# Kernel tuning notes

Measured on AMD Instinct MI355X. Metric: run time of the kernel, lower is better.

## Reference

```python
import jax, jax.numpy as jnp
import numpy as np

B_, S_, DM, DI, N_, R_, K_ = 2, 2048, 256, 512, 16, 32, 4
NB = 4  # 2 forward + 2 backward MambaBlocks


def setup_inputs() -> dict:
    key = jax.random.key(0)
    ks = jax.random.split(key, 16)
    def rn(k, shape, s=0.02):
        return jax.random.normal(k, shape, jnp.float32) * s
    A = jnp.log(jnp.arange(1, N_ + 1, dtype=jnp.float32))  # [N]
    return {
        'x': jax.random.normal(ks[0], (B_, S_, DM), jnp.float32),
        'in_w': rn(ks[1], (NB, DM, 2 * DI)),
        'conv_w': rn(ks[2], (NB, DI, K_), 0.3),
        'conv_b': jnp.zeros((NB, DI), jnp.float32),
        'A_log': jnp.broadcast_to(A, (NB, DI, N_)) + 0.0,
        'xd_w': rn(ks[3], (NB, DI, R_)),
        'xB_w': rn(ks[4], (NB, DI, N_)),
        'xC_w': rn(ks[5], (NB, DI, N_)),
        'dtp_w': rn(ks[6], (NB, R_, DI), R_ ** -0.5),
        'dtp_b': jax.random.uniform(ks[7], (NB, DI), jnp.float32,
                                    minval=jnp.log(0.001), maxval=jnp.log(0.1)),
        'D': jnp.ones((NB, DI), jnp.float32),
        'out_w': rn(ks[8], (NB, DI, DM)),
        'ln_g': jnp.ones((NB, DM), jnp.float32),
        'ln_b': jnp.zeros((NB, DM), jnp.float32),
        'merge_w': rn(ks[9], (2 * DM, DM)),
    }


def _layer_norm(x, g, b, eps=1e-5):
    m = jnp.mean(x, axis=-1, keepdims=True)
    v = jnp.mean(jnp.square(x - m), axis=-1, keepdims=True)
    return (x - m) * jax.lax.rsqrt(v + eps) * g + b


def _ssm_scan(dA, dBx, C):
    # dA, dBx: [B,S,DI,N]; C: [B,S,N] -> y: [B,S,DI]
    def step(h, inp):
        dA_t, dBx_t, C_t = inp
        h = dA_t * h + dBx_t                      # [B,DI,N]
        y = jnp.einsum('bdn,bn->bd', h, C_t)      # [B,DI]
        return h, y
    h0 = jnp.zeros(dA.shape[:1] + dA.shape[2:], dA.dtype)
    _, ys = jax.lax.scan(step, h0, (dA.transpose(1, 0, 2, 3),
                                    dBx.transpose(1, 0, 2, 3),
                                    C.transpose(1, 0, 2)))
    return ys.transpose(1, 0, 2)


def _mamba_block(x, in_w, conv_w, conv_b, A_log, xd_w, xB_w, xC_w,
                 dtp_w, dtp_b, D, out_w, g, b):
    res = x
    xn = _layer_norm(x, g, b)
    xz = xn @ in_w                                # [B,S,2*DI]
    xs, z = jnp.split(xz, 2, axis=-1)
    # causal depthwise conv: left pad K-1 (equals torch pad=K-1 then slice [:S])
    xc = jax.lax.conv_general_dilated(
        xs.transpose(0, 2, 1), conv_w[:, None, :], (1,), [(K_ - 1, 0)],
        dimension_numbers=('NCH', 'OIH', 'NCH'), feature_group_count=DI)
    xc = jax.nn.silu((xc + conv_b[None, :, None]).transpose(0, 2, 1))  # [B,S,DI]
    delta = jax.nn.softplus((xc @ xd_w) @ dtp_w + dtp_b)               # [B,S,DI]
    Bm = xc @ xB_w                                # [B,S,N]
    Cm = xc @ xC_w                                # [B,S,N]
    A = -jnp.exp(A_log)                           # [DI,N]
    dA = jnp.exp(delta[..., None] * A)            # [B,S,DI,N]
    dBx = (delta * xc)[..., None] * Bm[:, :, None, :]
    y = _ssm_scan(dA, dBx, Cm) + D * xc
    return (y * jax.nn.silu(z)) @ out_w + res


def reference(x, in_w, conv_w, conv_b, A_log, xd_w, xB_w, xC_w,
              dtp_w, dtp_b, D, out_w, ln_g, ln_b, merge_w):
    def blk(h, i):
        return _mamba_block(h, in_w[i], conv_w[i], conv_b[i], A_log[i],
                            xd_w[i], xB_w[i], xC_w[i], dtp_w[i], dtp_b[i],
                            D[i], out_w[i], ln_g[i], ln_b[i])
    fwd = blk(blk(x, 0), 1)
    bwd = blk(blk(x[:, ::-1], 2), 3)[:, ::-1]
    return jnp.concatenate([fwd, bwd], axis=-1) @ merge_w
```

## Files before the change

### kernel.cpp

```cpp
#include <hip/hip_runtime.h>

#define S_LEN 2048
#define DINNER 512
#define NCHUNK 64
#define CLEN 32

typedef unsigned short u16;
typedef short bf16x8 __attribute__((ext_vector_type(8)));
typedef unsigned short u16x8 __attribute__((ext_vector_type(8)));
typedef float f32x4 __attribute__((ext_vector_type(4)));

__device__ __forceinline__ float bf2f(u16 u) {
  unsigned int x = ((unsigned int)u) << 16;
  float f; __builtin_memcpy(&f, &x, 4); return f;
}
__device__ __forceinline__ u16 f2bf(float f) {
  unsigned int x; __builtin_memcpy(&x, &f, 4);
  return (u16)((x + 0x7FFFu + ((x >> 16) & 1u)) >> 16);
}
__device__ __forceinline__ float ldw(const void* p, size_t i, int isbf) {
  return isbf ? bf2f(((const u16*)p)[i]) : ((const float*)p)[i];
}
__device__ __forceinline__ float siluf(float x) { return x / (1.f + __expf(-x)); }
__device__ __forceinline__ float softplusf(float x) {
  if (x > 20.f) return x;
  return log1pf(__expf(x));
}

__global__ __launch_bounds__(256) void detect_kernel(const void* __restrict__ x,
                                                     int* __restrict__ flag) {
  __shared__ int cnt;
  if (threadIdx.x == 0) cnt = 0;
  __syncthreads();
  u16 u = ((const u16*)x)[2 * threadIdx.x];
  int e = (u >> 7) & 0xFF;
  if (e >= 0x60 && e <= 0x8F) atomicAdd(&cnt, 1);
  __syncthreads();
  if (threadIdx.x == 0) *flag = (cnt > 128) ? 1 : 0;
}

__global__ __launch_bounds__(256) void apack_kernel(
    const void* __restrict__ A_log, const int* __restrict__ pf, float* __restrict__ Acp)
{
  const int isbf = *pf;
  int idx = blockIdx.x * 256 + threadIdx.x;
  Acp[idx] = -__expf(ldw(A_log, (size_t)idx, isbf));
}

__global__ __launch_bounds__(256) void wpack_kernel(
    const void* __restrict__ src, const int* __restrict__ pf,
    u16* __restrict__ dst, int K, int N)
{
  const int isbf = *pf;
  __shared__ float tile[32][65];
  int nb64 = blockIdx.x, kb = blockIdx.y, mat = blockIdx.z;
  size_t so = (size_t)mat * K * N;
  int tid = threadIdx.x;
  int kk = tid >> 3, nseg = (tid & 7) * 8;
#pragma unroll
  for (int j = 0; j < 8; ++j)
    tile[kk][nseg + j] = ldw(src, so + (size_t)(kb * 32 + kk) * N + nb64 * 64 + nseg + j, isbf);
  __syncthreads();
  int cc = tid >> 6, i0 = (tid & 63) * 8;
  int q = i0 >> 7, nn = (i0 >> 3) & 15;
  u16 outv[8];
#pragma unroll
  for (int j = 0; j < 8; ++j) outv[j] = f2bf(tile[q * 8 + j][cc * 16 + nn]);
  size_t doff = (size_t)mat * K * N + ((size_t)(nb64 * 4 + cc) * (K >> 5) + kb) * 512 + i0;
  *(u16x8*)(dst + doff) = *(const u16x8*)outv;
}

__global__ __launch_bounds__(256) void wpack_cmb_kernel(
    const void* __restrict__ xdw, const void* __restrict__ dtpw,
    const void* __restrict__ xBw, const void* __restrict__ xCw,
    const int* __restrict__ pf, u16* __restrict__ dst)
{
  const int isbf = *pf;
  __shared__ float tile[32][65];
  int nb64 = blockIdx.x, kb = blockIdx.y, mat = blockIdx.z;
  int tid = threadIdx.x;
  if (nb64 < 8) {
    __shared__ float xd[32][33];
    __shared__ float wt[32][65];
    {
      int k = tid >> 3, j0 = (tid & 7) * 4;
#pragma unroll
      for (int j = 0; j < 4; ++j)
        xd[k][j0 + j] = ldw(xdw, (size_t)mat * 16384 + (size_t)(kb * 32 + k) * 32 + j0 + j, isbf);
      int jj = tid >> 3, n0l = (tid & 7) * 8;
#pragma unroll
      for (int n = 0; n < 8; ++n)
        wt[jj][n0l + n] = ldw(dtpw, (size_t)mat * 16384 + (size_t)jj * 512 + nb64 * 64 + n0l + n, isbf);
    }
    __syncthreads();
    for (int l = tid; l < 2048; l += 256) {
      int k = l >> 6, n = l & 63;
      float a = 0.f;
#pragma unroll
      for (int j = 0; j < 32; ++j) a += xd[k][j] * wt[j][n];
      tile[k][n] = a;
    }
  } else {
    for (int l = tid; l < 2048; l += 256) {
      int k = l >> 6, n = l & 63;
      int kg = kb * 32 + k;
      float v = 0.f;
      if (n < 16)      v = ldw(xBw, (size_t)mat * 8192 + (size_t)kg * 16 + n, isbf);
      else if (n < 32) v = ldw(xCw, (size_t)mat * 8192 + (size_t)kg * 16 + (n - 16), isbf);
      tile[k][n] = v;
    }
  }
  __syncthreads();
  int cc = tid >> 6, i0 = (tid & 63) * 8;
  int q = i0 >> 7, nn = (i0 >> 3) & 15;
  u16 outv[8];
#pragma unroll
  for (int j = 0; j < 8; ++j) outv[j] = f2bf(tile[q * 8 + j][cc * 16 + nn]);
  size_t doff = (size_t)mat * 294912 + ((size_t)(nb64 * 4 + cc) * 16 + kb) * 512 + i0;
  *(u16x8*)(dst + doff) = *(const u16x8*)outv;
}

__global__ __launch_bounds__(256) void ln_kernel(
    const void* __restrict__ x, const u16* __restrict__ obA, int it,
    const void* __restrict__ g, const void* __restrict__ bta,
    const int* __restrict__ pf, float* __restrict__ res, u16* __restrict__ xnb)
{
  const int isbf = *pf;
  int r = blockIdx.x;
  int tid = threadIdx.x;
  int chain = r >> 12, rr = r & 4095;
  int i = chain * 2 + it;
  size_t wo = (size_t)i * 256;
  float v;
  if (it == 0) {
    int b = rr >> 11, s = rr & 2047;
    int sr = chain ? (b * S_LEN + (S_LEN - 1 - s)) : rr;
    v = ldw(x, (size_t)sr * 256 + tid, isbf);
  } else {
    v = bf2f(obA[(size_t)r * 256 + tid]);
  }
  res[(size_t)r * 256 + tid] = v;
  float s1 = v, s2 = v * v;
#pragma unroll
  for (int o = 32; o > 0; o >>= 1) {
    s1 += __shfl_xor(s1, o, 64);
    s2 += __shfl_xor(s2, o, 64);
  }
  __shared__ float r1[4], r2[4];
  if ((tid & 63) == 0) { r1[tid >> 6] = s1; r2[tid >> 6] = s2; }
  __syncthreads();
  s1 = r1[0] + r1[1] + r1[2] + r1[3];
  s2 = r2[0] + r2[1] + r2[2] + r2[3];
  float mean = s1 * (1.f / 256.f);
  float var  = s2 * (1.f / 256.f) - mean * mean;
  float inv  = rsqrtf(var + 1e-5f);
  xnb[(size_t)r * 256 + tid] =
      f2bf((v - mean) * inv * ldw(g, wo + tid, isbf) + ldw(bta, wo + tid, isbf));
}

template<int OUTMODE>
__global__ __launch_bounds__(256) void gemm64(
    const u16* __restrict__ A, const u16* __restrict__ Wp, size_t woA, size_t woB, int mhalf,
    const float* __restrict__ res, void* __restrict__ Out, void* __restrict__ Out2,
    const void* __restrict__ bias, size_t boA, size_t boB,
    const int* __restrict__ pf, int N, int K, int nbx)
{
  const int isbf = *pf;
  __shared__ __align__(16) u16 Asb[2 * 64 * 32];
  __shared__ __align__(16) u16 Bsb[2 * 64 * 32];
  int tid = threadIdx.x;
  int gidx = blockIdx.x;
  int xcd = gidx & 7, rest = gidx >> 3;
  int nIdx = rest % nbx, mGrp = rest / nbx;
  int n0 = nIdx * 64, m0 = (xcd + (mGrp << 3)) * 64;
  size_t wo = (mhalf && m0 >= mhalf) ? woB : woA;
  int w = tid >> 6, lane = tid & 63;
  int q = lane >> 4, r = lane & 15;
  const int wm0 = (w >> 1) * 2, wn0 = (w & 1) * 2;
  const int kbs = K >> 5;
  f32x4 acc[2][2];
#pragma unroll
  for (int i = 0; i < 2; ++i)
#pragma unroll
    for (int j = 0; j < 2; ++j) acc[i][j] = (f32x4){0.f, 0.f, 0.f, 0.f};

  int sm = tid >> 2, sq = tid & 3;
  const u16* asrc = A + (size_t)(m0 + sm) * K + sq * 8;
  u16* adst = Asb + ((sm >> 4) * 4 + sq) * 128 + (sm & 15) * 8;
  int bnb = tid >> 6, binner = (tid & 63) * 8;
  u16* bdst = Bsb + bnb * 512 + binner;

  for (int k0 = 0; k0 < K; k0 += 64) {
    *(u16x8*)adst          = *(const u16x8*)(asrc + k0);
    *(u16x8*)(adst + 2048) = *(const u16x8*)(asrc + k0 + 32);
    const u16* bsrc = Wp + wo + ((size_t)((n0 >> 4) + bnb) * kbs + (k0 >> 5)) * 512 + binner;
    *(u16x8*)bdst          = *(const u16x8*)bsrc;
    *(u16x8*)(bdst + 2048) = *(const u16x8*)(bsrc + 512);
    __syncthreads();
#pragma unroll
    for (int ck = 0; ck < 2; ++ck) {
      const u16* Ab = Asb + ck * 2048;
      const u16* Bb = Bsb + ck * 2048;
      bf16x8 af[2], bfr[2];
#pragma unroll
      for (int i = 0; i < 2; ++i)
        af[i] = *(const bf16x8*)(Ab + ((wm0 + i) * 4 + q) * 128 + r * 8);
#pragma unroll
      for (int j = 0; j < 2; ++j)
        bfr[j] = *(const bf16x8*)(Bb + ((wn0 + j) * 4 + q) * 128 + r * 8);
#pragma unroll
      for (int i = 0; i < 2; ++i)
#pragma unroll
        for (int j = 0; j < 2; ++j)
          acc[i][j] = __builtin_amdgcn_mfma_f32_16x16x32_bf16(af[i], bfr[j], acc[i][j], 0, 0, 0);
    }
    __syncthreads();
  }
#pragma unroll
  for (int i = 0; i < 2; ++i) {
    int rowb = m0 + (wm0 + i) * 16 + q * 4;
#pragma unroll
    for (int j = 0; j < 2; ++j) {
      int col = n0 + (wn0 + j) * 16 + r;
#pragma unroll
      for (int t = 0; t < 4; ++t) {
        int row = rowb + t;
        float v = acc[i][j][t];
        if (OUTMODE == 2 || OUTMODE == 3) { if (res) v += res[(size_t)row * N + col]; }
        if (OUTMODE == 1) {
          size_t lidx = (size_t)row * N + col;
          if (isbf) ((u16*)Out)[lidx] = f2bf(v); else ((float*)Out)[lidx] = v;
        } else if (OUTMODE == 2) {
          ((u16*)Out)[(size_t)row * N + col] = f2bf(v);
        } else if (OUTMODE == 3) {
          int orow, cofx;
          if (row < 4096) { orow = row; cofx = 0; }
          else {
            int rr = row - 4096; int bb = rr >> 11, ss = rr & 2047;
            orow = bb * S_LEN + (S_LEN - 1 - ss); cofx = 256;
          }
          ((u16*)Out)[(size_t)orow * 512 + col + cofx] = f2bf(v);
        } else if (OUTMODE == 5) {
          if (col < 512) {
            float bv = ldw(bias, ((row < 4096) ? boA : boB) + col, isbf);
            ((u16*)Out)[(size_t)row * 512 + col] = f2bf(softplusf(v + bv));
          } else if (col < 544) {
            ((float*)Out2)[(size_t)row * 32 + (col - 512)] = v;
          }
        }
      }
    }
  }
}

__global__ __launch_bounds__(256) void conv_kernel(
    const u16* __restrict__ xzb, const void* __restrict__ cw, const void* __restrict__ cb,
    int it, const int* __restrict__ pf, u16* __restrict__ xcb)
{
  const int isbf = *pf;
  int idx = blockIdx.x * 256 + threadIdx.x;
  int r = idx >> 9, d = idx & 511;
  int chain = r >> 12, rr = r & 4095;
  int i = chain * 2 + it;
  size_t ow = (size_t)i * 2048, ob = (size_t)i * 512;
  int s = rr & 2047;
  float acc = ldw(cb, ob + d, isbf);
#pragma unroll
  for (int k = 0; k < 4; ++k) {
    int t = s - 3 + k;
    if (t >= 0)
      acc += ldw(cw, ow + (size_t)d * 4 + k, isbf) * bf2f(xzb[((size_t)(r + t - s) << 10) + d]);
  }
  xcb[idx] = f2bf(siluf(acc));
}

__global__ __launch_bounds__(256) void scan_p1_kernel(
    const u16* __restrict__ xcb, const u16* __restrict__ delb, const float* __restrict__ dBC,
    const float* __restrict__ Acp, int it, const int* __restrict__ pf,
    float* __restrict__ aggA, float* __restrict__ aggB)
{
  __shared__ float sb[32][16];
  __shared__ u16 sdu[32][64];
  __shared__ u16 sxu[32][64];
  int tid = threadIdx.x;
  int di = tid >> 2, ng = tid & 3;
  int d0 = blockIdx.x << 6;
  int c = blockIdx.y, seq = blockIdx.z;
  int chain = seq >> 1, bb = seq & 1;
  int row0 = chain * 4096 + bb * S_LEN + c * CLEN;
  int i = chain * 2 + it;
  {
    int t = tid >> 3, e0 = (tid & 7) * 8;
    *(u16x8*)&sdu[t][e0] = *(const u16x8*)(delb + (size_t)(row0 + t) * 512 + d0 + e0);
    *(u16x8*)&sxu[t][e0] = *(const u16x8*)(xcb + (size_t)(row0 + t) * 512 + d0 + e0);
  }
  if (tid < 128) {
    int t = tid >> 2, e0 = (tid & 3) * 4;
    *(f32x4*)&sb[t][e0] = *(const f32x4*)(dBC + (size_t)(row0 + t) * 32 + e0);
  }
  f32x4 Ac = *(const f32x4*)(Acp + ((size_t)i * 512 + d0 + di) * 16 + ng * 4);
  __syncthreads();
  float h[4] = {0.f, 0.f, 0.f, 0.f};
  float ap[4] = {1.f, 1.f, 1.f, 1.f};
#pragma unroll 8
  for (int t = 0; t < CLEN; ++t) {
    float de = bf2f(sdu[t][di]);
    float dx = de * bf2f(sxu[t][di]);
    f32x4 B = *(const f32x4*)&sb[t][ng * 4];
#pragma unroll
    for (int j = 0; j < 4; ++j) {
      float e = __expf(de * Ac[j]);
      h[j] = e * h[j] + dx * B[j];
      ap[j] *= e;
    }
  }
  size_t o = (((size_t)(seq * NCHUNK + c) * DINNER) + d0 + di) * 16 + ng * 4;
  *(f32x4*)(aggA + o) = (f32x4){ap[0], ap[1], ap[2], ap[3]};
  *(f32x4*)(aggB + o) = (f32x4){h[0], h[1], h[2], h[3]};
}

__global__ __launch_bounds__(256) void scan_prefix_kernel(
    const float* __restrict__ aggA, float* __restrict__ aggB)
{
  int idx = blockIdx.x * 256 + threadIdx.x;
  int n = idx & 15, d = (idx >> 4) & 511, seq = idx >> 13;
  float h = 0.f;
  for (int c = 0; c < NCHUNK; ++c) {
    size_t o = (((size_t)(seq * NCHUNK + c) * DINNER) + d) * 16 + n;
    float a = aggA[o], t = aggB[o];
    aggB[o] = h;
    h = a * h + t;
  }
}

__global__ __launch_bounds__(256) void scan_p3_kernel(
    const u16* __restrict__ xcb, const u16* __restrict__ delb, const float* __restrict__ dBC,
    const u16* __restrict__ xzb, const float* __restrict__ hpref,
    const float* __restrict__ Acp, const void* __restrict__ Dp,
    int it, const int* __restrict__ pf, u16* __restrict__ ymb)
{
  const int isbf = *pf;
  __shared__ float sbc[32][32];
  __shared__ float sy[32][64];
  __shared__ u16 sdu[32][64];
  __shared__ u16 sxu[32][64];
  __shared__ u16 szu[32][64];
  int tid = threadIdx.x;
  int di = tid >> 2, ng = tid & 3;
  int d0 = blockIdx.x << 6;
  int c = blockIdx.y, seq = blockIdx.z;
  int chain = seq >> 1, bb = seq & 1;
  int row0 = chain * 4096 + bb * S_LEN + c * CLEN;
  int i = chain * 2 + it;
  size_t oD = (size_t)i * 512;
  {
    int t = tid >> 3, e0 = (tid & 7) * 8;
    *(u16x8*)&sdu[t][e0] = *(const u16x8*)(delb + (size_t)(row0 + t) * 512 + d0 + e0);
    *(u16x8*)&sxu[t][e0] = *(const u16x8*)(xcb + (size_t)(row0 + t) * 512 + d0 + e0);
    *(u16x8*)&szu[t][e0] = *(const u16x8*)(xzb + ((size_t)(row0 + t) << 10) + 512 + d0 + e0);
  }
  {
    int t = tid >> 3, e0 = (tid & 7) * 4;
    *(f32x4*)&sbc[t][e0] = *(const f32x4*)(dBC + (size_t)(row0 + t) * 32 + e0);
  }
  f32x4 Ac = *(const f32x4*)(Acp + ((size_t)i * 512 + d0 + di) * 16 + ng * 4);
  float Dv = ldw(Dp, oD + d0 + di, isbf);
  float h[4];
  size_t o = (((size_t)(seq * NCHUNK + c) * DINNER) + d0 + di) * 16 + ng * 4;
  {
    f32x4 v = *(const f32x4*)(hpref + o);
    h[0] = v[0]; h[1] = v[1]; h[2] = v[2]; h[3] = v[3];
  }
  __syncthreads();
#pragma unroll 8
  for (int t = 0; t < CLEN; ++t) {
    float de = bf2f(sdu[t][di]);
    float xv = bf2f(sxu[t][di]);
    float dx = de * xv;
    f32x4 B = *(const f32x4*)&sbc[t][ng * 4];
    f32x4 C = *(const f32x4*)&sbc[t][16 + ng * 4];
    float yc = 0.f;
#pragma unroll
    for (int j = 0; j < 4; ++j) {
      float e = __expf(de * Ac[j]);
      h[j] = e * h[j] + dx * B[j];
      yc += h[j] * C[j];
    }
    yc += __shfl_xor(yc, 1, 64);
    yc += __shfl_xor(yc, 2, 64);
    if (ng == 0) sy[t][di] = yc + Dv * xv;
  }
  __syncthreads();
  int dcol = tid & 63;
#pragma unroll
  for (int k = 0; k < 8; ++k) {
    int t = (tid >> 6) + k * 4;
    float y = sy[t][dcol];
    float z = bf2f(szu[t][dcol]);
    ymb[(size_t)(row0 + t) * 512 + d0 + dcol] = f2bf(y * siluf(z));
  }
}

extern "C" void kernel_launch(void* const* d_in, const int* in_sizes, int n_in,
                              void* d_out, int out_size, void* d_ws, size_t ws_size,
                              hipStream_t stream)
{
  const void* x       = d_in[0];
  const void* in_w    = d_in[1];
  const void* conv_w  = d_in[2];
  const void* conv_b  = d_in[3];
  const void* A_log   = d_in[4];
  const void* xd_w    = d_in[5];
  const void* xB_w    = d_in[6];
  const void* xC_w    = d_in[7];
  const void* dtp_w   = d_in[8];
  const void* dtp_b   = d_in[9];
  const void* Dp      = d_in[10];
  const void* out_w   = d_in[11];
  const void* ln_g    = d_in[12];
  const void* ln_b    = d_in[13];
  const void* merge_w = d_in[14];

  float* ws    = (float*)d_ws;
  float* res   = ws;
  float* dBC   = res + (size_t)8192 * 256;
  float* aggA  = dBC + (size_t)8192 * 32;
  float* aggB  = aggA + (size_t)2097152;
  u16*   xz_bf = (u16*)(aggB + (size_t)2097152);
  u16*   xc_bf = xz_bf + (size_t)8192 * 1024;
  u16*   del_bf= xc_bf + (size_t)8192 * 512;
  u16*   Wp_in = del_bf + (size_t)8192 * 512;
  u16*   Wp_out= Wp_in + (size_t)4 * 262144;
  u16*   Wp_mg = Wp_out + (size_t)4 * 131072;
  u16*   Wp_cmb= Wp_mg + (size_t)131072;
  float* Acp   = (float*)(Wp_cmb + (size_t)4 * 294912);
  int*   flagp = (int*)(Acp + (size_t)4 * 8192);
  u16*   obA_bf= xz_bf;
  u16*   xn_bf = (u16*)aggA;
  u16*   ym_bf = (u16*)aggA;
  u16*   cat_bf= del_bf;

  dim3 blk(256);
  hipLaunchKernelGGL(detect_kernel, dim3(1), blk, 0, stream, x, flagp);
  hipLaunchKernelGGL(apack_kernel, dim3(128), blk, 0, stream, A_log, flagp, Acp);
  hipLaunchKernelGGL(wpack_kernel, dim3(16, 8, 4), blk, 0, stream, in_w, flagp, Wp_in, 256, 1024);
  hipLaunchKernelGGL(wpack_kernel, dim3(4, 16, 4), blk, 0, stream, out_w, flagp, Wp_out, 512, 256);
  hipLaunchKernelGGL(wpack_kernel, dim3(4, 16, 1), blk, 0, stream, merge_w, flagp, Wp_mg, 512, 256);
  hipLaunchKernelGGL(wpack_cmb_kernel, dim3(9, 16, 4), blk, 0, stream,
      xd_w, dtp_w, xB_w, xC_w, flagp, Wp_cmb);

  for (int it = 0; it < 2; ++it) {
    hipLaunchKernelGGL(ln_kernel, dim3(8192), blk, 0, stream,
        x, obA_bf, it, ln_g, ln_b, flagp, res, xn_bf);
    hipLaunchKernelGGL((gemm64<2>), dim3(16 * 128), blk, 0, stream,
        xn_bf, Wp_in, (size_t)it * 262144, (size_t)(2 + it) * 262144, 4096,
        (const float*)nullptr, (void*)xz_bf, (void*)nullptr,
        (const void*)nullptr, (size_t)0, (size_t)0, flagp, 1024, 256, 16);
    hipLaunchKernelGGL(conv_kernel, dim3(16384), blk, 0, stream,
        xz_bf, conv_w, conv_b, it, flagp, xc_bf);
    hipLaunchKernelGGL((gemm64<5>), dim3(9 * 128), blk, 0, stream,
        xc_bf, Wp_cmb, (size_t)it * 294912, (size_t)(2 + it) * 294912, 4096,
        (const float*)nullptr, (void*)del_bf, (void*)dBC,
        dtp_b, (size_t)it * 512, (size_t)(2 + it) * 512, flagp, 576, 512, 9);
    hipLaunchKernelGGL(scan_p1_kernel, dim3(8, NCHUNK, 4), blk, 0, stream,
        xc_bf, del_bf, dBC, Acp, it, flagp, aggA, aggB);
    hipLaunchKernelGGL(scan_prefix_kernel, dim3(128), blk, 0, stream, aggA, aggB);
    hipLaunchKernelGGL(scan_p3_kernel, dim3(8, NCHUNK, 4), blk, 0, stream,
        xc_bf, del_bf, dBC, xz_bf, aggB, Acp, Dp, it, flagp, ym_bf);
    if (it == 0) {
      hipLaunchKernelGGL((gemm64<2>), dim3(4 * 128), blk, 0, stream,
          ym_bf, Wp_out, (size_t)0, (size_t)2 * 131072, 4096,
          res, (void*)obA_bf, (void*)nullptr,
          (const void*)nullptr, (size_t)0, (size_t)0, flagp, 256, 512, 4);
    } else {
      hipLaunchKernelGGL((gemm64<3>), dim3(4 * 128), blk, 0, stream,
          ym_bf, Wp_out, (size_t)1 * 131072, (size_t)3 * 131072, 4096,
          res, (void*)cat_bf, (void*)nullptr,
          (const void*)nullptr, (size_t)0, (size_t)0, flagp, 256, 512, 4);
    }
  }
  hipLaunchKernelGGL((gemm64<1>), dim3(4 * 64), blk, 0, stream,
      cat_bf, Wp_mg, (size_t)0, (size_t)0, 0,
      (const float*)nullptr, d_out, (void*)nullptr,
      (const void*)nullptr, (size_t)0, (size_t)0, flagp, 256, 512, 4);
}
```

Baseline: 384.3 us.

## Use direct global-to-LDS loads in GEMM, vectorize conv, prefetch prefix scan

After: 432.0 us. 1.12x slower.

```diff
diff --git a/kernel.cpp b/kernel.cpp
--- a/kernel.cpp
+++ b/kernel.cpp
@@ -25,6 +25,12 @@
 __device__ __forceinline__ float softplusf(float x) {
   if (x > 20.f) return x;
   return log1pf(__expf(x));
+}
+
+typedef __attribute__((address_space(1))) const void gvoid_t;
+typedef __attribute__((address_space(3))) void lvoid_t;
+__device__ __forceinline__ void glds16(const u16* g, u16* l) {
+  __builtin_amdgcn_global_load_lds((gvoid_t*)g, (lvoid_t*)l, 16, 0, 0);
 }
 
 __global__ __launch_bounds__(256) void detect_kernel(const void* __restrict__ x,
@@ -184,18 +190,17 @@
 #pragma unroll
     for (int j = 0; j < 2; ++j) acc[i][j] = (f32x4){0.f, 0.f, 0.f, 0.f};
 
-  int sm = tid >> 2, sq = tid & 3;
-  const u16* asrc = A + (size_t)(m0 + sm) * K + sq * 8;
-  u16* adst = Asb + ((sm >> 4) * 4 + sq) * 128 + (sm & 15) * 8;
-  int bnb = tid >> 6, binner = (tid & 63) * 8;
-  u16* bdst = Bsb + bnb * 512 + binner;
+  const u16* asrc = A + (size_t)(m0 + (w << 4) + (lane & 15)) * K + ((lane >> 4) << 3);
+  u16* albase = Asb + w * 512;
+  const size_t bbase = wo + (size_t)((n0 >> 4) + w) * kbs * 512 + lane * 8;
+  u16* blbase = Bsb + w * 512;
 
   for (int k0 = 0; k0 < K; k0 += 64) {
-    *(u16x8*)adst          = *(const u16x8*)(asrc + k0);
-    *(u16x8*)(adst + 2048) = *(const u16x8*)(asrc + k0 + 32);
-    const u16* bsrc = Wp + wo + ((size_t)((n0 >> 4) + bnb) * kbs + (k0 >> 5)) * 512 + binner;
-    *(u16x8*)bdst          = *(const u16x8*)bsrc;
-    *(u16x8*)(bdst + 2048) = *(const u16x8*)(bsrc + 512);
+    glds16(asrc + k0,        albase);
+    glds16(asrc + k0 + 32,   albase + 2048);
+    const u16* bsrc = Wp + bbase + (size_t)(k0 >> 5) * 512;
+    glds16(bsrc,       blbase);
+    glds16(bsrc + 512, blbase + 2048);
     __syncthreads();
 #pragma unroll
     for (int ck = 0; ck < 2; ++ck) {
@@ -259,19 +264,29 @@
 {
   const int isbf = *pf;
   int idx = blockIdx.x * 256 + threadIdx.x;
-  int r = idx >> 9, d = idx & 511;
+  int r = idx >> 6, dg = idx & 63;
+  int d0 = dg << 3;
   int chain = r >> 12, rr = r & 4095;
   int i = chain * 2 + it;
   size_t ow = (size_t)i * 2048, ob = (size_t)i * 512;
   int s = rr & 2047;
-  float acc = ldw(cb, ob + d, isbf);
+  float acc[8];
+#pragma unroll
+  for (int j = 0; j < 8; ++j) acc[j] = ldw(cb, ob + d0 + j, isbf);
 #pragma unroll
   for (int k = 0; k < 4; ++k) {
     int t = s - 3 + k;
-    if (t >= 0)
-      acc += ldw(cw, ow + (size_t)d * 4 + k, isbf) * bf2f(xzb[((size_t)(r + t - s) << 10) + d]);
-  }
-  xcb[idx] = f2bf(siluf(acc));
+    if (t >= 0) {
+      u16x8 xv = *(const u16x8*)(xzb + (((size_t)(r + t - s)) << 10) + d0);
+#pragma unroll
+      for (int j = 0; j < 8; ++j)
+        acc[j] += ldw(cw, ow + (size_t)(d0 + j) * 4 + k, isbf) * bf2f(xv[j]);
+    }
+  }
+  u16 outv[8];
+#pragma unroll
+  for (int j = 0; j < 8; ++j) outv[j] = f2bf(siluf(acc[j]));
+  *(u16x8*)(xcb + ((size_t)r << 9) + d0) = *(const u16x8*)outv;
 }
 
 __global__ __launch_bounds__(256) void scan_p1_kernel(
@@ -319,17 +334,22 @@
   *(f32x4*)(aggB + o) = (f32x4){h[0], h[1], h[2], h[3]};
 }
 
-__global__ __launch_bounds__(256) void scan_prefix_kernel(
+__global__ __launch_bounds__(64) void scan_prefix_kernel(
     const float* __restrict__ aggA, float* __restrict__ aggB)
 {
-  int idx = blockIdx.x * 256 + threadIdx.x;
+  int idx = blockIdx.x * 64 + threadIdx.x;
   int n = idx & 15, d = (idx >> 4) & 511, seq = idx >> 13;
+  size_t o = (((size_t)(seq * NCHUNK) * DINNER) + d) * 16 + n;
+  float a = aggA[o], t = aggB[o];
   float h = 0.f;
   for (int c = 0; c < NCHUNK; ++c) {
-    size_t o = (((size_t)(seq * NCHUNK + c) * DINNER) + d) * 16 + n;
-    float a = aggA[o], t = aggB[o];
+    size_t on = o + (size_t)DINNER * 16;
+    float an = 0.f, tn = 0.f;
+    if (c + 1 < NCHUNK) { an = aggA[on]; tn = aggB[on]; }
     aggB[o] = h;
     h = a * h + t;
+    a = an; t = tn;
+    o = on;
   }
 }
 
@@ -456,7 +476,7 @@
         xn_bf, Wp_in, (size_t)it * 262144, (size_t)(2 + it) * 262144, 4096,
         (const float*)nullptr, (void*)xz_bf, (void*)nullptr,
         (const void*)nullptr, (size_t)0, (size_t)0, flagp, 1024, 256, 16);
-    hipLaunchKernelGGL(conv_kernel, dim3(16384), blk, 0, stream,
+    hipLaunchKernelGGL(conv_kernel, dim3(2048), blk, 0, stream,
         xz_bf, conv_w, conv_b, it, flagp, xc_bf);
     hipLaunchKernelGGL((gemm64<5>), dim3(9 * 128), blk, 0, stream,
         xc_bf, Wp_cmb, (size_t)it * 294912, (size_t)(2 + it) * 294912, 4096,
@@ -464,7 +484,7 @@
         dtp_b, (size_t)it * 512, (size_t)(2 + it) * 512, flagp, 576, 512, 9);
     hipLaunchKernelGGL(scan_p1_kernel, dim3(8, NCHUNK, 4), blk, 0, stream,
         xc_bf, del_bf, dBC, Acp, it, flagp, aggA, aggB);
-    hipLaunchKernelGGL(scan_prefix_kernel, dim3(128), blk, 0, stream, aggA, aggB);
+    hipLaunchKernelGGL(scan_prefix_kernel, dim3(512), dim3(64), 0, stream, aggA, aggB);
     hipLaunchKernelGGL(scan_p3_kernel, dim3(8, NCHUNK, 4), blk, 0, stream,
         xc_bf, del_bf, dBC, xz_bf, aggB, Acp, Dp, it, flagp, ym_bf);
     if (it == 0) {
```
